# Kernel tuning notes

Measured on AMD Instinct MI355X. Metric: run time of the kernel, lower is better.

## Reference

```python
import jax, jax.numpy as jnp
import numpy as np

N_NODES = 100000


def gcn_layer(x, edge_index, W, b, num_nodes):
    # GCNConv (PyG): h = x @ W; add self-loops; symmetric deg^-1/2 norm; scatter-add; + bias
    h = x @ W  # [N, out]
    loops = jnp.arange(num_nodes, dtype=edge_index.dtype)
    src = jnp.concatenate([edge_index[0], loops])
    dst = jnp.concatenate([edge_index[1], loops])
    deg = jax.ops.segment_sum(jnp.ones(src.shape[0], dtype=h.dtype), dst,
                              num_segments=num_nodes)  # includes self-loop, so deg >= 1
    dis = jax.lax.rsqrt(deg)  # deg^-1/2
    norm = dis[src] * dis[dst]  # [E+N]
    msg = h[src] * norm[:, None]  # gather + scale
    out = jax.ops.segment_sum(msg, dst, num_segments=num_nodes)  # scatter-add
    return out + b


def setup_inputs() -> dict:
    key = jax.random.key(0)
    k1, k2, k3, k4 = jax.random.split(key, 4)
    num_feature, hidden, num_label = 512, 16, 40
    n_edges = 3200000
    x = jax.random.normal(k1, (N_NODES, num_feature), dtype=jnp.float32)
    edge_index = jax.random.randint(k2, (2, n_edges), 0, N_NODES, dtype=jnp.int64)
    # Glorot-style init for weights
    W1 = jax.random.normal(k3, (num_feature, hidden), dtype=jnp.float32) / np.sqrt(num_feature)
    b1 = jnp.zeros((hidden,), dtype=jnp.float32)
    W2 = jax.random.normal(k4, (hidden, num_label), dtype=jnp.float32) / np.sqrt(hidden)
    b2 = jnp.zeros((num_label,), dtype=jnp.float32)
    return {"x": x, "edge_index": edge_index, "W1": W1, "b1": b1, "W2": W2, "b2": b2}


def reference(x, edge_index, W1, b1, W2, b2):
    h = gcn_layer(x, edge_index, W1, b1, N_NODES)
    h = jax.nn.relu(h)
    # dropout is identity in eval mode
    h = gcn_layer(h, edge_index, W2, b2, N_NODES)
    return jax.nn.log_softmax(h, axis=1)
```

## Files before the change

kernel.cpp:

```cpp
#include <hip/hip_runtime.h>
#include <math.h>

#define N_NODES 100000
#define N_EDGES 3200000
#define F_IN    512
#define H1      16
#define H2      40

#define NB      196
#define BSH     9
#define BMASK   511
#define B1      512
#define EPB     6250

__global__ void detect_idx_kernel(const int* __restrict__ ei, int* __restrict__ flag)
{
    if (threadIdx.x == 0 && blockIdx.x == 0) {
        int all_zero = 1;
        for (int i = 0; i < 64; ++i)
            if (ei[2 * i + 1] != 0) { all_zero = 0; break; }
        *flag = all_zero;
    }
}

__device__ __forceinline__ int edge_src(const void* ei, int e, int is64)
{
    return is64 ? (int)((const long long*)ei)[e] : ((const int*)ei)[e];
}
__device__ __forceinline__ int edge_dst(const void* ei, int e, int is64)
{
    return is64 ? (int)((const long long*)ei)[N_EDGES + e]
                : ((const int*)ei)[N_EDGES + e];
}

__global__ __launch_bounds__(256) void hist_kernel(
    const void* __restrict__ ei, const int* __restrict__ flag,
    int* __restrict__ cntoff)
{
    __shared__ int h[NB];
    if (threadIdx.x < NB) h[threadIdx.x] = 0;
    __syncthreads();
    const int is64 = *flag;
    const int e0 = blockIdx.x * EPB;
    for (int i = threadIdx.x; i < EPB; i += 256) {
        int e = e0 + i;
        if (e < N_EDGES) atomicAdd(&h[edge_dst(ei, e, is64) >> BSH], 1);
    }
    __syncthreads();
    if (threadIdx.x < NB) cntoff[blockIdx.x * NB + threadIdx.x] = h[threadIdx.x];
}

__global__ __launch_bounds__(256) void scanblk_kernel(
    int* __restrict__ cntoff, int* __restrict__ bstart)
{
    const int lane   = threadIdx.x & 63;
    const int bucket = blockIdx.x * 4 + (threadIdx.x >> 6);
    if (bucket >= NB) return;
    int run = 0;
    #pragma unroll
    for (int c = 0; c < B1 / 64; ++c) {
        const int i = c * 64 + lane;
        const int v = cntoff[i * NB + bucket];
        int s = v;
        #pragma unroll
        for (int off = 1; off < 64; off <<= 1) {
            int t = __shfl_up(s, off, 64);
            if (lane >= off) s += t;
        }
        cntoff[i * NB + bucket] = run + (s - v);
        run += __shfl(s, 63, 64);
    }
    if (lane == 0) bstart[bucket] = run;
}

__global__ __launch_bounds__(256) void scanb_kernel(int* __restrict__ bstart)
{
    __shared__ int s[256];
    const int t = threadIdx.x;
    const int v = (t < NB) ? bstart[t] : 0;
    s[t] = v;
    __syncthreads();
    for (int off = 1; off < 256; off <<= 1) {
        int tv = (t >= off) ? s[t - off] : 0;
        __syncthreads();
        s[t] += tv;
        __syncthreads();
    }
    if (t < NB) bstart[t] = s[t] - v;
    if (t == NB - 1) bstart[NB] = s[t];
}

__global__ __launch_bounds__(256) void scatter_bucket_kernel(
    const void* __restrict__ ei, const int* __restrict__ flag,
    const int* __restrict__ cntoff, const int* __restrict__ bstart,
    int* __restrict__ packed)
{
    __shared__ int cur[NB];
    if (threadIdx.x < NB)
        cur[threadIdx.x] = cntoff[blockIdx.x * NB + threadIdx.x] + bstart[threadIdx.x];
    __syncthreads();
    const int is64 = *flag;
    const int e0 = blockIdx.x * EPB;
    for (int i = threadIdx.x; i < EPB; i += 256) {
        int e = e0 + i;
        if (e >= N_EDGES) break;
        const int s = edge_src(ei, e, is64);
        const int d = edge_dst(ei, e, is64);
        const int b = d >> BSH;
        const int pos = atomicAdd(&cur[b], 1);
        packed[pos] = (s << BSH) | (d & BMASK);
    }
}

__global__ __launch_bounds__(512) void bucket_csr_kernel(
    const int* __restrict__ packed, const int* __restrict__ bstart,
    int* __restrict__ deg, int* __restrict__ row_end, int* __restrict__ csr)
{
    __shared__ int hist[512];
    __shared__ int off2[512];
    __shared__ int stmp[256];
    const int b    = blockIdx.x;
    const int tid  = threadIdx.x;
    const int base = bstart[b];
    const int m    = bstart[b + 1] - base;

    hist[tid] = 0;
    __syncthreads();
    for (int i = tid; i < m; i += 512)
        atomicAdd(&hist[packed[base + i] & BMASK], 1);
    __syncthreads();

    int h0 = 0, h1 = 0;
    if (tid < 256) {
        h0 = hist[2 * tid];
        h1 = hist[2 * tid + 1];
        stmp[tid] = h0 + h1;
    }
    __syncthreads();
    for (int off = 1; off < 256; off <<= 1) {
        int t = 0;
        if (tid < 256 && tid >= off) t = stmp[tid - off];
        __syncthreads();
        if (tid < 256) stmp[tid] += t;
        __syncthreads();
    }
    if (tid < 256) {
        const int ex2 = stmp[tid] - (h0 + h1);
        off2[2 * tid]     = ex2;
        off2[2 * tid + 1] = ex2 + h0;
        const int g0 = (b << BSH) + 2 * tid;
        const int g1 = g0 + 1;
        if (g0 < N_NODES) { deg[g0] = h0; row_end[g0] = base + ex2 + h0; }
        if (g1 < N_NODES) { deg[g1] = h1; row_end[g1] = base + ex2 + h0 + h1; }
    }
    __syncthreads();
    for (int i = tid; i < m; i += 512) {
        const int p = packed[base + i];
        const int pos = atomicAdd(&off2[p & BMASK], 1);
        csr[base + pos] = p >> BSH;
    }
}

__global__ __launch_bounds__(256) void gemm1_kernel(
    const float* __restrict__ x, const float* __restrict__ W1,
    const int* __restrict__ deg, float* __restrict__ hs1,
    float* __restrict__ dis, int n)
{
    const int r = blockIdx.x * 256 + threadIdx.x;
    if (r >= n) return;

    const float4* xr = (const float4*)(x + (size_t)r * F_IN);
    float acc[H1];
    #pragma unroll
    for (int j = 0; j < H1; ++j) acc[j] = 0.f;

    #pragma unroll 2
    for (int k4 = 0; k4 < F_IN / 4; ++k4) {
        const float4 xv = xr[k4];
        const float* wk = W1 + k4 * 4 * H1;
        #pragma unroll
        for (int j = 0; j < H1; ++j)
            acc[j] += xv.x * wk[j] + xv.y * wk[H1 + j]
                    + xv.z * wk[2 * H1 + j] + xv.w * wk[3 * H1 + j];
    }

    const float dv = rsqrtf((float)deg[r] + 1.0f);
    dis[r] = dv;
    float4* o = (float4*)(hs1 + (size_t)r * H1);
    #pragma unroll
    for (int q = 0; q < 4; ++q) {
        float4 v;
        v.x = acc[4 * q + 0] * dv;
        v.y = acc[4 * q + 1] * dv;
        v.z = acc[4 * q + 2] * dv;
        v.w = acc[4 * q + 3] * dv;
        o[q] = v;
    }
}

template <int FUSE_L1>
__global__ __launch_bounds__(256) void pull16_kernel(
    const int* __restrict__ row_end, const int* __restrict__ csr,
    const float* __restrict__ rows, const float* __restrict__ dis,
    const float* __restrict__ b1, float* __restrict__ out, int n)
{
    int t = blockIdx.x * 256 + threadIdx.x;
    int g = t >> 2;
    int q = t & 3;
    if (g >= n) return;
    int beg = (g == 0) ? 0 : row_end[g - 1];
    int end = row_end[g];
    float4 acc = make_float4(0.f, 0.f, 0.f, 0.f);
    for (int i = beg; i < end; ++i) {
        int s = csr[i];
        float4 v = ((const float4*)(rows + (size_t)s * H1))[q];
        acc.x += v.x; acc.y += v.y; acc.z += v.z; acc.w += v.w;
    }
    if (FUSE_L1) {
        const float dv = dis[g];
        float4 h = ((const float4*)(rows + (size_t)g * H1))[q];
        float4 bq = ((const float4*)b1)[q];
        acc.x = dv * fmaxf(dv * (acc.x + h.x) + bq.x, 0.f);
        acc.y = dv * fmaxf(dv * (acc.y + h.y) + bq.y, 0.f);
        acc.z = dv * fmaxf(dv * (acc.z + h.z) + bq.z, 0.f);
        acc.w = dv * fmaxf(dv * (acc.w + h.w) + bq.w, 0.f);
    }
    ((float4*)(out + (size_t)g * H1))[q] = acc;
}

__global__ __launch_bounds__(256) void epi_kernel(
    const float* __restrict__ agg2, const float* __restrict__ c,
    const float* __restrict__ W2, const float* __restrict__ b2,
    const float* __restrict__ dis, float* __restrict__ out, int n)
{
    __shared__ float w[H1 * H2];
    for (int t = threadIdx.x; t < H1 * H2; t += 256) w[t] = W2[t];
    __syncthreads();

    const int row  = blockIdx.x * 4 + (threadIdx.x >> 6);
    if (row >= n) return;
    const int lane = threadIdx.x & 63;

    float tv = 0.f;
    if (lane < H1)
        tv = agg2[(size_t)row * H1 + lane] + c[(size_t)row * H1 + lane];

    const float dv = dis[row];
    float val = -INFINITY;
    if (lane < H2) {
        float s = 0.f;
        #pragma unroll
        for (int k = 0; k < H1; ++k) {
            float tk = __shfl(tv, k, 64);
            s += tk * w[k * H2 + lane];
        }
        val = dv * s + b2[lane];
    }
    float m = val;
    #pragma unroll
    for (int off = 32; off > 0; off >>= 1) m = fmaxf(m, __shfl_xor(m, off, 64));
    float ex = (lane < H2) ? __expf(val - m) : 0.f;
    #pragma unroll
    for (int off = 32; off > 0; off >>= 1) ex += __shfl_xor(ex, off, 64);
    if (lane < H2) out[(size_t)row * H2 + lane] = val - m - logf(ex);
}

extern "C" void kernel_launch(void* const* d_in, const int* in_sizes, int n_in,
                              void* d_out, int out_size, void* d_ws, size_t ws_size,
                              hipStream_t stream)
{
    const float* x   = (const float*)d_in[0];
    const void*  ei  = d_in[1];
    const float* W1  = (const float*)d_in[2];
    const float* b1  = (const float*)d_in[3];
    const float* W2  = (const float*)d_in[4];
    const float* b2  = (const float*)d_in[5];
    float*       out = (float*)d_out;

    int*   base    = (int*)d_ws;
    int*   flag    = base;
    int*   deg     = base + 16;
    int*   row_end = deg + N_NODES;
    int*   bstart  = row_end + N_NODES;
    int*   cntoff  = bstart + 256;
    float* dis     = (float*)(cntoff + B1 * NB);
    int*   csr     = (int*)(dis + N_NODES);
    int*   packed  = csr + N_EDGES;
    float* hs1     = (float*)packed;
    float* c       = hs1 + (size_t)N_NODES * H1;
    float* agg2    = hs1;

    detect_idx_kernel<<<1, 64, 0, stream>>>((const int*)ei, flag);

    hist_kernel<<<B1, 256, 0, stream>>>(ei, flag, cntoff);
    scanblk_kernel<<<(NB + 3) / 4, 256, 0, stream>>>(cntoff, bstart);
    scanb_kernel<<<1, 256, 0, stream>>>(bstart);
    scatter_bucket_kernel<<<B1, 256, 0, stream>>>(ei, flag, cntoff, bstart, packed);
    bucket_csr_kernel<<<NB, 512, 0, stream>>>(packed, bstart, deg, row_end, csr);

    gemm1_kernel<<<(N_NODES + 255) / 256, 256, 0, stream>>>(x, W1, deg, hs1, dis, N_NODES);

    const int PB = (N_NODES * 4 + 255) / 256;
    pull16_kernel<1><<<PB, 256, 0, stream>>>(row_end, csr, hs1, dis, b1, c, N_NODES);
    pull16_kernel<0><<<PB, 256, 0, stream>>>(row_end, csr, c, dis, b1, agg2, N_NODES);

    epi_kernel<<<(N_NODES + 3) / 4, 256, 0, stream>>>(agg2, c, W2, b2, dis, out, N_NODES);
}
```

Baseline: 296.1 us.

## Use smaller destination buckets and compute two rows per thread in gemm1

Halves the destination bucket width, from 512 to 256 nodes, which roughly doubles the bucket count to 391. The hist, scan, scatter and bucket-CSR kernels are adjusted to match, and the per-bucket CSR pass is simplified to a direct 256-entry scan. Separately, gemm1 now processes two rows per thread and loads four float4s at a time, so each W1 load is reused across two rows. The trade-offs are more global scan entries and lower thread counts in gemm1, with higher register pressure per thread.

Result: slower. 579.3 us (+95.7%).

```diff
diff --git a/kernel.cpp b/kernel.cpp
--- a/kernel.cpp
+++ b/kernel.cpp
@@ -7,9 +7,9 @@
 #define H1      16
 #define H2      40
 
-#define NB      196
-#define BSH     9
-#define BMASK   511
+#define NB      391
+#define BSH     8
+#define BMASK   255
 #define B1      512
 #define EPB     6250
 
@@ -38,7 +38,7 @@
     int* __restrict__ cntoff)
 {
     __shared__ int h[NB];
-    if (threadIdx.x < NB) h[threadIdx.x] = 0;
+    for (int i = threadIdx.x; i < NB; i += 256) h[i] = 0;
     __syncthreads();
     const int is64 = *flag;
     const int e0 = blockIdx.x * EPB;
@@ -47,7 +47,8 @@
         if (e < N_EDGES) atomicAdd(&h[edge_dst(ei, e, is64) >> BSH], 1);
     }
     __syncthreads();
-    if (threadIdx.x < NB) cntoff[blockIdx.x * NB + threadIdx.x] = h[threadIdx.x];
+    for (int i = threadIdx.x; i < NB; i += 256)
+        cntoff[blockIdx.x * NB + i] = h[i];
 }
 
 __global__ __launch_bounds__(256) void scanblk_kernel(
@@ -73,14 +74,14 @@
     if (lane == 0) bstart[bucket] = run;
 }
 
-__global__ __launch_bounds__(256) void scanb_kernel(int* __restrict__ bstart)
-{
-    __shared__ int s[256];
+__global__ __launch_bounds__(512) void scanb_kernel(int* __restrict__ bstart)
+{
+    __shared__ int s[512];
     const int t = threadIdx.x;
     const int v = (t < NB) ? bstart[t] : 0;
     s[t] = v;
     __syncthreads();
-    for (int off = 1; off < 256; off <<= 1) {
+    for (int off = 1; off < 512; off <<= 1) {
         int tv = (t >= off) ? s[t - off] : 0;
         __syncthreads();
         s[t] += tv;
@@ -96,8 +97,8 @@
     int* __restrict__ packed)
 {
     __shared__ int cur[NB];
-    if (threadIdx.x < NB)
-        cur[threadIdx.x] = cntoff[blockIdx.x * NB + threadIdx.x] + bstart[threadIdx.x];
+    for (int i = threadIdx.x; i < NB; i += 256)
+        cur[i] = cntoff[blockIdx.x * NB + i] + bstart[i];
     __syncthreads();
     const int is64 = *flag;
     const int e0 = blockIdx.x * EPB;
@@ -116,85 +117,94 @@
     const int* __restrict__ packed, const int* __restrict__ bstart,
     int* __restrict__ deg, int* __restrict__ row_end, int* __restrict__ csr)
 {
-    __shared__ int hist[512];
-    __shared__ int off2[512];
-    __shared__ int stmp[256];
+    __shared__ int hist[256];
+    __shared__ int off[256];
     const int b    = blockIdx.x;
     const int tid  = threadIdx.x;
     const int base = bstart[b];
     const int m    = bstart[b + 1] - base;
 
-    hist[tid] = 0;
+    if (tid < 256) hist[tid] = 0;
     __syncthreads();
     for (int i = tid; i < m; i += 512)
         atomicAdd(&hist[packed[base + i] & BMASK], 1);
     __syncthreads();
 
-    int h0 = 0, h1 = 0;
+    int v = 0;
+    if (tid < 256) { v = hist[tid]; off[tid] = v; }
+    __syncthreads();
+    for (int o = 1; o < 256; o <<= 1) {
+        int t2 = 0;
+        if (tid < 256 && tid >= o) t2 = off[tid - o];
+        __syncthreads();
+        if (tid < 256) off[tid] += t2;
+        __syncthreads();
+    }
     if (tid < 256) {
-        h0 = hist[2 * tid];
-        h1 = hist[2 * tid + 1];
-        stmp[tid] = h0 + h1;
-    }
-    __syncthreads();
-    for (int off = 1; off < 256; off <<= 1) {
-        int t = 0;
-        if (tid < 256 && tid >= off) t = stmp[tid - off];
-        __syncthreads();
-        if (tid < 256) stmp[tid] += t;
-        __syncthreads();
-    }
-    if (tid < 256) {
-        const int ex2 = stmp[tid] - (h0 + h1);
-        off2[2 * tid]     = ex2;
-        off2[2 * tid + 1] = ex2 + h0;
-        const int g0 = (b << BSH) + 2 * tid;
-        const int g1 = g0 + 1;
-        if (g0 < N_NODES) { deg[g0] = h0; row_end[g0] = base + ex2 + h0; }
-        if (g1 < N_NODES) { deg[g1] = h1; row_end[g1] = base + ex2 + h0 + h1; }
+        const int g = (b << BSH) + tid;
+        if (g < N_NODES) { deg[g] = v; row_end[g] = base + off[tid]; }
+        off[tid] -= v;
     }
     __syncthreads();
     for (int i = tid; i < m; i += 512) {
         const int p = packed[base + i];
-        const int pos = atomicAdd(&off2[p & BMASK], 1);
+        const int pos = atomicAdd(&off[p & BMASK], 1);
         csr[base + pos] = p >> BSH;
     }
 }
 
-__global__ __launch_bounds__(256) void gemm1_kernel(
+__global__ __launch_bounds__(128) void gemm1_kernel(
     const float* __restrict__ x, const float* __restrict__ W1,
     const int* __restrict__ deg, float* __restrict__ hs1,
     float* __restrict__ dis, int n)
 {
-    const int r = blockIdx.x * 256 + threadIdx.x;
-    if (r >= n) return;
-
-    const float4* xr = (const float4*)(x + (size_t)r * F_IN);
-    float acc[H1];
-    #pragma unroll
-    for (int j = 0; j < H1; ++j) acc[j] = 0.f;
-
-    #pragma unroll 2
-    for (int k4 = 0; k4 < F_IN / 4; ++k4) {
-        const float4 xv = xr[k4];
-        const float* wk = W1 + k4 * 4 * H1;
-        #pragma unroll
-        for (int j = 0; j < H1; ++j)
-            acc[j] += xv.x * wk[j] + xv.y * wk[H1 + j]
-                    + xv.z * wk[2 * H1 + j] + xv.w * wk[3 * H1 + j];
-    }
-
-    const float dv = rsqrtf((float)deg[r] + 1.0f);
-    dis[r] = dv;
-    float4* o = (float4*)(hs1 + (size_t)r * H1);
+    const int t  = blockIdx.x * 128 + threadIdx.x;
+    const int r0 = 2 * t;
+    if (r0 >= n) return;
+    const int r1 = r0 + 1;
+    const float4* xa = (const float4*)(x + (size_t)r0 * F_IN);
+    const float4* xb = (const float4*)(x + (size_t)r1 * F_IN);
+
+    float acca[H1], accb[H1];
+    #pragma unroll
+    for (int j = 0; j < H1; ++j) { acca[j] = 0.f; accb[j] = 0.f; }
+
+    for (int kb = 0; kb < F_IN / 4; kb += 4) {
+        float4 va[4], vb[4];
+        #pragma unroll
+        for (int u = 0; u < 4; ++u) va[u] = xa[kb + u];
+        #pragma unroll
+        for (int u = 0; u < 4; ++u) vb[u] = xb[kb + u];
+        #pragma unroll
+        for (int u = 0; u < 4; ++u) {
+            const float* wk = W1 + (size_t)(kb + u) * 4 * H1;
+            #pragma unroll
+            for (int j = 0; j < H1; ++j) {
+                const float w0 = wk[j];
+                const float w1 = wk[H1 + j];
+                const float w2 = wk[2 * H1 + j];
+                const float w3 = wk[3 * H1 + j];
+                acca[j] += va[u].x * w0 + va[u].y * w1 + va[u].z * w2 + va[u].w * w3;
+                accb[j] += vb[u].x * w0 + vb[u].y * w1 + vb[u].z * w2 + vb[u].w * w3;
+            }
+        }
+    }
+
+    const float da = rsqrtf((float)deg[r0] + 1.0f);
+    const float db = rsqrtf((float)deg[r1] + 1.0f);
+    dis[r0] = da;
+    dis[r1] = db;
+    float4* oa = (float4*)(hs1 + (size_t)r0 * H1);
+    float4* ob = (float4*)(hs1 + (size_t)r1 * H1);
     #pragma unroll
     for (int q = 0; q < 4; ++q) {
-        float4 v;
-        v.x = acc[4 * q + 0] * dv;
-        v.y = acc[4 * q + 1] * dv;
-        v.z = acc[4 * q + 2] * dv;
-        v.w = acc[4 * q + 3] * dv;
-        o[q] = v;
+        float4 u, w;
+        u.x = acca[4 * q + 0] * da; u.y = acca[4 * q + 1] * da;
+        u.z = acca[4 * q + 2] * da; u.w = acca[4 * q + 3] * da;
+        w.x = accb[4 * q + 0] * db; w.y = accb[4 * q + 1] * db;
+        w.z = accb[4 * q + 2] * db; w.w = accb[4 * q + 3] * db;
+        oa[q] = u;
+        ob[q] = w;
     }
 }
 
@@ -282,7 +292,7 @@
     int*   deg     = base + 16;
     int*   row_end = deg + N_NODES;
     int*   bstart  = row_end + N_NODES;
-    int*   cntoff  = bstart + 256;
+    int*   cntoff  = bstart + 512;
     float* dis     = (float*)(cntoff + B1 * NB);
     int*   csr     = (int*)(dis + N_NODES);
     int*   packed  = csr + N_EDGES;
@@ -294,11 +304,11 @@
 
     hist_kernel<<<B1, 256, 0, stream>>>(ei, flag, cntoff);
     scanblk_kernel<<<(NB + 3) / 4, 256, 0, stream>>>(cntoff, bstart);
-    scanb_kernel<<<1, 256, 0, stream>>>(bstart);
+    scanb_kernel<<<1, 512, 0, stream>>>(bstart);
     scatter_bucket_kernel<<<B1, 256, 0, stream>>>(ei, flag, cntoff, bstart, packed);
     bucket_csr_kernel<<<NB, 512, 0, stream>>>(packed, bstart, deg, row_end, csr);
 
-    gemm1_kernel<<<(N_NODES + 255) / 256, 256, 0, stream>>>(x, W1, deg, hs1, dis, N_NODES);
+    gemm1_kernel<<<(N_NODES / 2 + 127) / 128, 128, 0, stream>>>(x, W1, deg, hs1, dis, N_NODES);
 
     const int PB = (N_NODES * 4 + 255) / 256;
     pull16_kernel<1><<<PB, 256, 0, stream>>>(row_end, csr, hs1, dis, b1, c, N_NODES);
```
